# Kernel tuning notes

Hardware: AMD Instinct MI355X
Metric: run time of the kernel (lower is better)

The kernel has to match this reference:

```python
import jax, jax.numpy as jnp
import numpy as np

B, CIN, COUT, K, H, W, MAPPING_DIM = 8, 32, 32, 3, 512, 512, 1024


def setup_inputs() -> dict:
    key = jax.random.key(0)
    k1, k2, k3, k4 = jax.random.split(key, 4)
    x = jax.random.normal(k1, (B, CIN, H, W), dtype=jnp.float32)
    w = jax.random.normal(k2, (B, MAPPING_DIM), dtype=jnp.float32)
    kernel = jax.random.normal(k3, (COUT, CIN, K, K), dtype=jnp.float32) * 0.02
    style_w = jax.random.normal(k4, (CIN, MAPPING_DIM), dtype=jnp.float32) * (1.0 / np.sqrt(MAPPING_DIM))
    style_b = jnp.zeros((CIN,), dtype=jnp.float32)
    return {"x": x, "w": w, "kernel": kernel, "style_w": style_w, "style_b": style_b}


def reference(x, w, kernel, style_w, style_b):
    # style = Linear(MAPPING_DIM -> in_channels)(w)  -> [b, cin]
    style = jnp.einsum('bm,cm->bc', w, style_w) + style_b
    # Per-sample modulated kernel (kernel * style broadcast over input channel)
    # is mathematically identical to scaling input channels then a shared conv:
    # conv(x, kernel * style_b) == conv(x * style_b, kernel). This fuses the
    # modulation into the activations, avoiding the [b*cout, cin, k, k] tensor.
    xm = x * style[:, :, None, None]  # [b, cin, h, w]
    pad = K // 2
    out = jax.lax.conv_general_dilated(
        xm, kernel,
        window_strides=(1, 1),
        padding=[(pad, pad), (pad, pad)],
        dimension_numbers=('NCHW', 'OIHW', 'NCHW'),
    )  # [b, cout, h, w]
    return out
```

## Files before the change

### kernel.cpp

```cpp
#include <hip/hip_runtime.h>
#include <hip/hip_bf16.h>


typedef short  short8 __attribute__((ext_vector_type(8)));
typedef float  f32x4  __attribute__((ext_vector_type(4)));

#define TH 8
#define TW 32
#define XCOLS (TH ? (TW + 2) : 0)
#define CPAD 40

static __device__ inline unsigned short f2bf(float f) {
    unsigned int u = __float_as_uint(f);
    unsigned int r = (u + 0x7fffu + ((u >> 16) & 1u)) >> 16;
    return (unsigned short)r;
}

__global__ void style_kernel(const float* __restrict__ w, const float* __restrict__ sw,
                             const float* __restrict__ sb, float* __restrict__ style) {
    int wid  = (blockIdx.x * 256 + threadIdx.x) >> 6;
    int lane = threadIdx.x & 63;
    int b = wid >> 5, ci = wid & 31;
    const float* wp = w  + b  * 1024;
    const float* sp = sw + ci * 1024;
    float s = 0.f;
    #pragma unroll
    for (int i = 0; i < 16; ++i) s += wp[lane + 64 * i] * sp[lane + 64 * i];
    #pragma unroll
    for (int off = 32; off; off >>= 1) s += __shfl_down(s, off, 64);
    if (lane == 0) style[b * 32 + ci] = s + sb[ci];
}

__global__ void wprep_kernel(const float* __restrict__ kern, const float* __restrict__ style,
                             unsigned short* __restrict__ wfrag) {
    int tid = blockIdx.x * 256 + threadIdx.x;
    if (tid >= 8 * 9216) return;
    int b    = tid / 9216;
    int rem  = tid % 9216;
    int off  = rem >> 10;
    int r2   = rem & 1023;
    int half = r2 >> 9;
    int lane = (r2 >> 3) & 63;
    int j    = r2 & 7;
    int cout = half * 16 + (lane & 15);
    int cin  = (lane >> 4) * 8 + j;
    int kh = off / 3, kw = off % 3;
    float v = kern[(cout * 32 + cin) * 9 + kh * 3 + kw] * style[b * 32 + cin];
    wfrag[tid] = f2bf(v);
}

__global__ __launch_bounds__(256, 4) void conv_kernel(const float* __restrict__ x,
                                                      const unsigned short* __restrict__ wfrag,
                                                      float* __restrict__ out) {
    __shared__ unsigned short xs[(TH + 2) * XCOLS * CPAD];

    const int b  = blockIdx.z;
    const int h0 = blockIdx.y * TH;
    const int w0 = blockIdx.x * TW;
    const int t    = threadIdx.x;
    const int lane = t & 63, wave = t >> 6;

    short8 wreg[9][2];
    const unsigned short* wf = wfrag + b * 9216;
    #pragma unroll
    for (int off = 0; off < 9; ++off)
        #pragma unroll
        for (int hf = 0; hf < 2; ++hf)
            wreg[off][hf] = *(const short8*)(wf + ((off * 2 + hf) * 64 + lane) * 8);

    const float* xb = x + (size_t)b * 8388608;
    for (int tt = t; tt < 1600; tt += 256) {
        int col4 = tt % 10;
        int tmp  = tt / 10;
        int row  = tmp % 10;
        int cp   = tmp / 10;
        int gh   = h0 - 1 + row;
        int gw0  = w0 - 4 + col4 * 4;
        f32x4 a = {0.f, 0.f, 0.f, 0.f};
        f32x4 c = {0.f, 0.f, 0.f, 0.f};
        if ((unsigned)gh < 512u && (unsigned)gw0 <= 508u) {
            const float* p = xb + cp * 2 * 262144 + gh * 512 + gw0;
            a = *(const f32x4*)p;
            c = *(const f32x4*)(p + 262144);
        }
        #pragma unroll
        for (int e = 0; e < 4; ++e) {
            int xcol = col4 * 4 + e - 3;
            if ((unsigned)xcol < (unsigned)XCOLS) {
                float2 fp = make_float2(a[e], c[e]);
                __hip_bfloat162 h2 = __float22bfloat162_rn(fp);
                *(unsigned int*)&xs[(row * XCOLS + xcol) * CPAD + cp * 2] = *(unsigned int*)&h2;
            }
        }
    }
    __syncthreads();

    const int n  = lane & 15;
    const int kg = lane >> 4;
    float* ob = out + (size_t)b * 8388608;

    #pragma unroll 1
    for (int g = 0; g < 4; ++g) {
        const int r   = wave * 2 + (g >> 1);
        const int c16 = (g & 1) * 16;
        f32x4 acc0 = {0.f, 0.f, 0.f, 0.f};
        f32x4 acc1 = {0.f, 0.f, 0.f, 0.f};
        #pragma unroll
        for (int kh = 0; kh < 3; ++kh) {
            #pragma unroll
            for (int kw = 0; kw < 3; ++kw) {
                const short8 afrag =
                    *(const short8*)&xs[((r + kh) * XCOLS + c16 + kw + n) * CPAD + kg * 8];
                const int off = kh * 3 + kw;
                acc0 = __builtin_amdgcn_mfma_f32_16x16x32_bf16(afrag, wreg[off][0], acc0, 0, 0, 0);
                acc1 = __builtin_amdgcn_mfma_f32_16x16x32_bf16(afrag, wreg[off][1], acc1, 0, 0, 0);
            }
        }
        const int gh = h0 + r;
        const int gw = w0 + c16 + kg * 4;
        float* p0 = ob + (size_t)n * 262144 + gh * 512 + gw;
        *(f32x4*)p0 = acc0;
        *(f32x4*)(p0 + 16 * 262144) = acc1;
    }
}

extern "C" void kernel_launch(void* const* d_in, const int* in_sizes, int n_in,
                              void* d_out, int out_size, void* d_ws, size_t ws_size,
                              hipStream_t stream) {
    const float* x    = (const float*)d_in[0];
    const float* w    = (const float*)d_in[1];
    const float* kern = (const float*)d_in[2];
    const float* sw   = (const float*)d_in[3];
    const float* sb   = (const float*)d_in[4];
    float* out = (float*)d_out;

    float*          style = (float*)d_ws;
    unsigned short* wfrag = (unsigned short*)((char*)d_ws + 1024);

    style_kernel<<<64, 256, 0, stream>>>(w, sw, sb, style);
    wprep_kernel<<<288, 256, 0, stream>>>(kern, style, wfrag);
    conv_kernel<<<dim3(512 / TW, 512 / TH, 8), 256, 0, stream>>>(x, wfrag, out);
}
```

Before: 506.5 us.

## Stream rows through a shared-memory ring buffer with prefetch in conv kernel

Each conv block now covers a 64-row by 32-column strip and walks down it eight rows at a time. The next eight input rows are prefetched into registers while MFMA runs on the current rows, then written into a 16-row ring buffer in shared memory, so the halo rows are reused between steps instead of reloaded. The block grows to 512 threads, with each wave pair splitting the output channels. Blocks are remapped to interleave batches, outputs use nontemporal stores, and the style and weight-prep kernels are fused into a single 8-block launch. In exchange there are fewer blocks (1024) and extra barriers, and the prep kernel runs on very few blocks.

```diff
diff --git a/kernel.cpp b/kernel.cpp
--- a/kernel.cpp
+++ b/kernel.cpp
@@ -5,10 +5,9 @@
 typedef short  short8 __attribute__((ext_vector_type(8)));
 typedef float  f32x4  __attribute__((ext_vector_type(4)));
 
-#define TH 8
-#define TW 32
-#define XCOLS (TH ? (TW + 2) : 0)
-#define CPAD 40
+#define XCOLS 34
+#define CPAD  40
+#define NRING 16
 
 static __device__ inline unsigned short f2bf(float f) {
     unsigned int u = __float_as_uint(f);
@@ -16,111 +15,185 @@
     return (unsigned short)r;
 }
 
-__global__ void style_kernel(const float* __restrict__ w, const float* __restrict__ sw,
-                             const float* __restrict__ sb, float* __restrict__ style) {
-    int wid  = (blockIdx.x * 256 + threadIdx.x) >> 6;
-    int lane = threadIdx.x & 63;
-    int b = wid >> 5, ci = wid & 31;
-    const float* wp = w  + b  * 1024;
-    const float* sp = sw + ci * 1024;
-    float s = 0.f;
+__global__ __launch_bounds__(256) void prep_kernel(const float* __restrict__ w,
+                                                   const float* __restrict__ sw,
+                                                   const float* __restrict__ sb,
+                                                   const float* __restrict__ kern,
+                                                   unsigned short* __restrict__ wfrag) {
+    __shared__ float sstyle[32];
+    const int b = blockIdx.x;
+    const int t = threadIdx.x, lane = t & 63, wave = t >> 6;
+    const float* wp = w + b * 1024;
     #pragma unroll
-    for (int i = 0; i < 16; ++i) s += wp[lane + 64 * i] * sp[lane + 64 * i];
+    for (int i = 0; i < 8; ++i) {
+        const int ci = wave * 8 + i;
+        const float* sp = sw + ci * 1024;
+        float s = 0.f;
+        #pragma unroll
+        for (int k = 0; k < 16; ++k) s += wp[lane + 64 * k] * sp[lane + 64 * k];
+        #pragma unroll
+        for (int off = 32; off; off >>= 1) s += __shfl_down(s, off, 64);
+        if (lane == 0) sstyle[ci] = s + sb[ci];
+    }
+    __syncthreads();
+    unsigned short* wfb = wfrag + b * 9216;
     #pragma unroll
-    for (int off = 32; off; off >>= 1) s += __shfl_down(s, off, 64);
-    if (lane == 0) style[b * 32 + ci] = s + sb[ci];
-}
-
-__global__ void wprep_kernel(const float* __restrict__ kern, const float* __restrict__ style,
-                             unsigned short* __restrict__ wfrag) {
-    int tid = blockIdx.x * 256 + threadIdx.x;
-    if (tid >= 8 * 9216) return;
-    int b    = tid / 9216;
-    int rem  = tid % 9216;
-    int off  = rem >> 10;
-    int r2   = rem & 1023;
-    int half = r2 >> 9;
-    int lane = (r2 >> 3) & 63;
-    int j    = r2 & 7;
-    int cout = half * 16 + (lane & 15);
-    int cin  = (lane >> 4) * 8 + j;
-    int kh = off / 3, kw = off % 3;
-    float v = kern[(cout * 32 + cin) * 9 + kh * 3 + kw] * style[b * 32 + cin];
-    wfrag[tid] = f2bf(v);
-}
-
-__global__ __launch_bounds__(256, 4) void conv_kernel(const float* __restrict__ x,
+    for (int k = 0; k < 36; ++k) {
+        const int f = t + 256 * k;
+        const int off = f >> 10, r2 = f & 1023;
+        const int half = r2 >> 9, ln = (r2 >> 3) & 63, j = r2 & 7;
+        const int cout = half * 16 + (ln & 15);
+        const int cin  = (ln >> 4) * 8 + j;
+        const int kh = off / 3, kw = off % 3;
+        wfb[f] = f2bf(kern[(cout * 32 + cin) * 9 + kh * 3 + kw] * sstyle[cin]);
+    }
+}
+
+__global__ __launch_bounds__(512, 4) void conv_kernel(const float* __restrict__ x,
                                                       const unsigned short* __restrict__ wfrag,
                                                       float* __restrict__ out) {
-    __shared__ unsigned short xs[(TH + 2) * XCOLS * CPAD];
-
-    const int b  = blockIdx.z;
-    const int h0 = blockIdx.y * TH;
-    const int w0 = blockIdx.x * TW;
-    const int t    = threadIdx.x;
+    __shared__ unsigned short xs[NRING * XCOLS * CPAD];
+
+    const int p = blockIdx.x;
+    const int q = (p & 7) * 128 + (p >> 3);
+    const int b  = q >> 7;
+    const int tg = (q >> 4) & 7;
+    const int tw = q & 15;
+    const int w0 = tw * 32;
+    const int hbase = tg * 64;
+
+    const int t = threadIdx.x;
     const int lane = t & 63, wave = t >> 6;
-
-    short8 wreg[9][2];
-    const unsigned short* wf = wfrag + b * 9216;
-    #pragma unroll
-    for (int off = 0; off < 9; ++off)
-        #pragma unroll
-        for (int hf = 0; hf < 2; ++hf)
-            wreg[off][hf] = *(const short8*)(wf + ((off * 2 + hf) * 64 + lane) * 8);
+    const int hf = wave & 1;
+    const int ws = wave >> 1;
+    const int n  = lane & 15, kg = lane >> 4;
+
+    short8 wreg[9];
+    {
+        const unsigned short* wf = wfrag + b * 9216;
+        #pragma unroll
+        for (int off = 0; off < 9; ++off)
+            wreg[off] = *(const short8*)(wf + ((off * 2 + hf) * 64 + lane) * 8);
+    }
 
     const float* xb = x + (size_t)b * 8388608;
-    for (int tt = t; tt < 1600; tt += 256) {
-        int col4 = tt % 10;
-        int tmp  = tt / 10;
-        int row  = tmp % 10;
-        int cp   = tmp / 10;
-        int gh   = h0 - 1 + row;
-        int gw0  = w0 - 4 + col4 * 4;
-        f32x4 a = {0.f, 0.f, 0.f, 0.f};
-        f32x4 c = {0.f, 0.f, 0.f, 0.f};
-        if ((unsigned)gh < 512u && (unsigned)gw0 <= 508u) {
-            const float* p = xb + cp * 2 * 262144 + gh * 512 + gw0;
-            a = *(const f32x4*)p;
-            c = *(const f32x4*)(p + 262144);
-        }
-        #pragma unroll
-        for (int e = 0; e < 4; ++e) {
-            int xcol = col4 * 4 + e - 3;
-            if ((unsigned)xcol < (unsigned)XCOLS) {
-                float2 fp = make_float2(a[e], c[e]);
-                __hip_bfloat162 h2 = __float22bfloat162_rn(fp);
-                *(unsigned int*)&xs[(row * XCOLS + xcol) * CPAD + cp * 2] = *(unsigned int*)&h2;
+    float*       ob = out + (size_t)b * 8388608;
+
+    {
+        f32x4 va[4], vc[4];
+        #pragma unroll
+        for (int u = 0; u < 4; ++u) {
+            const int tt = t + 512 * u;
+            va[u] = (f32x4){0.f, 0.f, 0.f, 0.f};
+            vc[u] = (f32x4){0.f, 0.f, 0.f, 0.f};
+            if (tt < 1600) {
+                const int col4 = tt % 10;
+                const int row  = (tt / 10) % 10;
+                const int cp   = tt / 100;
+                const int gh   = hbase - 1 + row;
+                const int gw0  = w0 - 4 + col4 * 4;
+                if ((unsigned)gh < 512u && (unsigned)gw0 <= 508u) {
+                    const float* ptr = xb + cp * 2 * 262144 + gh * 512 + gw0;
+                    va[u] = *(const f32x4*)ptr;
+                    vc[u] = *(const f32x4*)(ptr + 262144);
+                }
+            }
+        }
+        #pragma unroll
+        for (int u = 0; u < 4; ++u) {
+            const int tt = t + 512 * u;
+            if (tt < 1600) {
+                const int col4 = tt % 10;
+                const int row  = (tt / 10) % 10;
+                const int cp   = tt / 100;
+                const int prow = (row + 15) & 15;
+                #pragma unroll
+                for (int e = 0; e < 4; ++e) {
+                    const int xcol = col4 * 4 + e - 3;
+                    if ((unsigned)xcol < (unsigned)XCOLS) {
+                        float2 fp = make_float2(va[u][e], vc[u][e]);
+                        __hip_bfloat162 h2 = __float22bfloat162_rn(fp);
+                        *(unsigned int*)&xs[(prow * XCOLS + xcol) * CPAD + cp * 2] =
+                            *(unsigned int*)&h2;
+                    }
+                }
             }
         }
     }
     __syncthreads();
 
-    const int n  = lane & 15;
-    const int kg = lane >> 4;
-    float* ob = out + (size_t)b * 8388608;
-
     #pragma unroll 1
-    for (int g = 0; g < 4; ++g) {
-        const int r   = wave * 2 + (g >> 1);
-        const int c16 = (g & 1) * 16;
-        f32x4 acc0 = {0.f, 0.f, 0.f, 0.f};
-        f32x4 acc1 = {0.f, 0.f, 0.f, 0.f};
-        #pragma unroll
-        for (int kh = 0; kh < 3; ++kh) {
+    for (int it = 0; it < 8; ++it) {
+        f32x4 va[3], vc[3];
+        const bool more = (it < 7);
+        if (more) {
+            const int grow0 = hbase + it * 8 + 9;
             #pragma unroll
-            for (int kw = 0; kw < 3; ++kw) {
-                const short8 afrag =
-                    *(const short8*)&xs[((r + kh) * XCOLS + c16 + kw + n) * CPAD + kg * 8];
-                const int off = kh * 3 + kw;
-                acc0 = __builtin_amdgcn_mfma_f32_16x16x32_bf16(afrag, wreg[off][0], acc0, 0, 0, 0);
-                acc1 = __builtin_amdgcn_mfma_f32_16x16x32_bf16(afrag, wreg[off][1], acc1, 0, 0, 0);
-            }
-        }
-        const int gh = h0 + r;
-        const int gw = w0 + c16 + kg * 4;
-        float* p0 = ob + (size_t)n * 262144 + gh * 512 + gw;
-        *(f32x4*)p0 = acc0;
-        *(f32x4*)(p0 + 16 * 262144) = acc1;
+            for (int u = 0; u < 3; ++u) {
+                const int tt = t + 512 * u;
+                va[u] = (f32x4){0.f, 0.f, 0.f, 0.f};
+                vc[u] = (f32x4){0.f, 0.f, 0.f, 0.f};
+                if (tt < 1280) {
+                    const int col4 = tt % 10;
+                    const int row  = (tt / 10) % 8;
+                    const int cp   = tt / 80;
+                    const int gh   = grow0 + row;
+                    const int gw0  = w0 - 4 + col4 * 4;
+                    if ((unsigned)gh < 512u && (unsigned)gw0 <= 508u) {
+                        const float* ptr = xb + cp * 2 * 262144 + gh * 512 + gw0;
+                        va[u] = *(const f32x4*)ptr;
+                        vc[u] = *(const f32x4*)(ptr + 262144);
+                    }
+                }
+            }
+        }
+
+        const int base = it * 8;
+        #pragma unroll
+        for (int g = 0; g < 4; ++g) {
+            const int r   = ws * 2 + (g >> 1);
+            const int c16 = (g & 1) * 16;
+            f32x4 acc = {0.f, 0.f, 0.f, 0.f};
+            #pragma unroll
+            for (int kh = 0; kh < 3; ++kh) {
+                const int prow = (base + r + kh - 1) & 15;
+                #pragma unroll
+                for (int kw = 0; kw < 3; ++kw) {
+                    const short8 afrag =
+                        *(const short8*)&xs[(prow * XCOLS + c16 + kw + n) * CPAD + kg * 8];
+                    acc = __builtin_amdgcn_mfma_f32_16x16x32_bf16(afrag, wreg[kh * 3 + kw],
+                                                                  acc, 0, 0, 0);
+                }
+            }
+            const int gh = hbase + base + r;
+            float* p0 = ob + (size_t)(hf * 16 + n) * 262144 + gh * 512 + (w0 + c16 + kg * 4);
+            __builtin_nontemporal_store(acc, (f32x4*)p0);
+        }
+        __syncthreads();
+
+        if (more) {
+            #pragma unroll
+            for (int u = 0; u < 3; ++u) {
+                const int tt = t + 512 * u;
+                if (tt < 1280) {
+                    const int col4 = tt % 10;
+                    const int row  = (tt / 10) % 8;
+                    const int cp   = tt / 80;
+                    const int prow = (it * 8 + 9 + row) & 15;
+                    #pragma unroll
+                    for (int e = 0; e < 4; ++e) {
+                        const int xcol = col4 * 4 + e - 3;
+                        if ((unsigned)xcol < (unsigned)XCOLS) {
+                            float2 fp = make_float2(va[u][e], vc[u][e]);
+                            __hip_bfloat162 h2 = __float22bfloat162_rn(fp);
+                            *(unsigned int*)&xs[(prow * XCOLS + xcol) * CPAD + cp * 2] =
+                                *(unsigned int*)&h2;
+                        }
+                    }
+                }
+            }
+            __syncthreads();
+        }
     }
 }
 
@@ -134,10 +207,8 @@
     const float* sb   = (const float*)d_in[4];
     float* out = (float*)d_out;
 
-    float*          style = (float*)d_ws;
-    unsigned short* wfrag = (unsigned short*)((char*)d_ws + 1024);
-
-    style_kernel<<<64, 256, 0, stream>>>(w, sw, sb, style);
-    wprep_kernel<<<288, 256, 0, stream>>>(kern, style, wfrag);
-    conv_kernel<<<dim3(512 / TW, 512 / TH, 8), 256, 0, stream>>>(x, wfrag, out);
-}
+    unsigned short* wfrag = (unsigned short*)d_ws;
+
+    prep_kernel<<<8, 256, 0, stream>>>(w, sw, sb, kern, wfrag);
+    conv_kernel<<<1024, 512, 0, stream>>>(x, wfrag, out);
+}
```

Measured after the change: 509.6 us. No clear change (+0.6%).

## Pre-transpose input to NHWC bf16 and convolve directly from global memory

Applied to the files above, without the earlier changes.

Adds a pass that converts x into a channels-last bf16 copy (in workspace, or in the spare upper half of the output buffer when workspace is small). The conv kernel then drops its shared-memory staging and reads A fragments straight from the NHWC buffer, with each wave reusing loaded rows for two output rows and owning one half of the output channels. The style and weight-prep kernels are merged into one launch. This trades an extra full read and write of x for contiguous channel loads and no LDS tile or barrier, and the fallback path relies on ordering batches so output writes do not overwrite staged inputs still to be read.

```diff
diff --git a/kernel.cpp b/kernel.cpp
--- a/kernel.cpp
+++ b/kernel.cpp
@@ -5,10 +5,7 @@
 typedef short  short8 __attribute__((ext_vector_type(8)));
 typedef float  f32x4  __attribute__((ext_vector_type(4)));
 
-#define TH 8
-#define TW 32
-#define XCOLS (TH ? (TW + 2) : 0)
-#define CPAD 40
+struct XtBases { unsigned short* p[8]; };
 
 static __device__ inline unsigned short f2bf(float f) {
     unsigned int u = __float_as_uint(f);
@@ -16,111 +13,122 @@
     return (unsigned short)r;
 }
 
-__global__ void style_kernel(const float* __restrict__ w, const float* __restrict__ sw,
-                             const float* __restrict__ sb, float* __restrict__ style) {
-    int wid  = (blockIdx.x * 256 + threadIdx.x) >> 6;
-    int lane = threadIdx.x & 63;
-    int b = wid >> 5, ci = wid & 31;
-    const float* wp = w  + b  * 1024;
-    const float* sp = sw + ci * 1024;
-    float s = 0.f;
+__global__ __launch_bounds__(256) void prep_kernel(const float* __restrict__ w,
+                                                   const float* __restrict__ sw,
+                                                   const float* __restrict__ sb,
+                                                   const float* __restrict__ kern,
+                                                   unsigned short* __restrict__ wfrag) {
+    __shared__ float sstyle[32];
+    const int b = blockIdx.x;
+    const int t = threadIdx.x, lane = t & 63, wave = t >> 6;
+    const float* wp = w + b * 1024;
     #pragma unroll
-    for (int i = 0; i < 16; ++i) s += wp[lane + 64 * i] * sp[lane + 64 * i];
+    for (int i = 0; i < 8; ++i) {
+        const int ci = wave * 8 + i;
+        const float* sp = sw + ci * 1024;
+        float s = 0.f;
+        #pragma unroll
+        for (int k = 0; k < 16; ++k) s += wp[lane + 64 * k] * sp[lane + 64 * k];
+        #pragma unroll
+        for (int off = 32; off; off >>= 1) s += __shfl_down(s, off, 64);
+        if (lane == 0) sstyle[ci] = s + sb[ci];
+    }
+    __syncthreads();
+    unsigned short* wfb = wfrag + b * 9216;
     #pragma unroll
-    for (int off = 32; off; off >>= 1) s += __shfl_down(s, off, 64);
-    if (lane == 0) style[b * 32 + ci] = s + sb[ci];
+    for (int k = 0; k < 36; ++k) {
+        const int f = t + 256 * k;
+        const int off = f >> 10, r2 = f & 1023;
+        const int half = r2 >> 9, ln = (r2 >> 3) & 63, j = r2 & 7;
+        const int cout = half * 16 + (ln & 15);
+        const int cin  = (ln >> 4) * 8 + j;
+        const int kh = off / 3, kw = off % 3;
+        wfb[f] = f2bf(kern[(cout * 32 + cin) * 9 + kh * 3 + kw] * sstyle[cin]);
+    }
 }
 
-__global__ void wprep_kernel(const float* __restrict__ kern, const float* __restrict__ style,
-                             unsigned short* __restrict__ wfrag) {
-    int tid = blockIdx.x * 256 + threadIdx.x;
-    if (tid >= 8 * 9216) return;
-    int b    = tid / 9216;
-    int rem  = tid % 9216;
-    int off  = rem >> 10;
-    int r2   = rem & 1023;
-    int half = r2 >> 9;
-    int lane = (r2 >> 3) & 63;
-    int j    = r2 & 7;
-    int cout = half * 16 + (lane & 15);
-    int cin  = (lane >> 4) * 8 + j;
-    int kh = off / 3, kw = off % 3;
-    float v = kern[(cout * 32 + cin) * 9 + kh * 3 + kw] * style[b * 32 + cin];
-    wfrag[tid] = f2bf(v);
+__global__ __launch_bounds__(256) void xt_kernel(const float* __restrict__ x, XtBases xb) {
+    const int b  = blockIdx.z;
+    const int h  = blockIdx.y;
+    const int w0 = blockIdx.x * 256;
+    const int t   = threadIdx.x;
+    const int px4 = t & 63;
+    const int c8  = t >> 6;
+    const float* xp = x + (size_t)b * 8388608 + h * 512 + (w0 + px4 * 4);
+    f32x4 v[8];
+    #pragma unroll
+    for (int j = 0; j < 8; ++j)
+        v[j] = *(const f32x4*)(xp + (size_t)(c8 * 8 + j) * 262144);
+    unsigned short* o = xb.p[b] + ((size_t)(h * 512 + w0 + px4 * 4) * 32 + c8 * 8);
+    #pragma unroll
+    for (int e = 0; e < 4; ++e) {
+        uint4 d;
+        __hip_bfloat162 h0 = __float22bfloat162_rn(make_float2(v[0][e], v[1][e]));
+        __hip_bfloat162 h1 = __float22bfloat162_rn(make_float2(v[2][e], v[3][e]));
+        __hip_bfloat162 h2 = __float22bfloat162_rn(make_float2(v[4][e], v[5][e]));
+        __hip_bfloat162 h3 = __float22bfloat162_rn(make_float2(v[6][e], v[7][e]));
+        d.x = *(unsigned int*)&h0; d.y = *(unsigned int*)&h1;
+        d.z = *(unsigned int*)&h2; d.w = *(unsigned int*)&h3;
+        *(uint4*)(o + e * 32) = d;
+    }
 }
 
-__global__ __launch_bounds__(256, 4) void conv_kernel(const float* __restrict__ x,
+__global__ __launch_bounds__(256, 4) void conv_kernel(XtBases xb,
                                                       const unsigned short* __restrict__ wfrag,
-                                                      float* __restrict__ out) {
-    __shared__ unsigned short xs[(TH + 2) * XCOLS * CPAD];
+                                                      float* __restrict__ out, int b0) {
+    const int b  = b0 + blockIdx.z;
+    const int h0 = blockIdx.y * 4;
+    const int w0 = blockIdx.x * 32;
+    const int t = threadIdx.x, lane = t & 63, wave = t >> 6;
+    const int hf = wave & 1, rp = wave >> 1;
+    const int n = lane & 15, kg = lane >> 4;
 
-    const int b  = blockIdx.z;
-    const int h0 = blockIdx.y * TH;
-    const int w0 = blockIdx.x * TW;
-    const int t    = threadIdx.x;
-    const int lane = t & 63, wave = t >> 6;
+    short8 wreg[9];
+    {
+        const unsigned short* wf = wfrag + b * 9216;
+        #pragma unroll
+        for (int off = 0; off < 9; ++off)
+            wreg[off] = *(const short8*)(wf + ((off * 2 + hf) * 64 + lane) * 8);
+    }
 
-    short8 wreg[9][2];
-    const unsigned short* wf = wfrag + b * 9216;
+    const unsigned short* xt = xb.p[b];
+    float* ob = out + (size_t)b * 8388608;
+    const int r0 = h0 + rp * 2;
+
     #pragma unroll
-    for (int off = 0; off < 9; ++off)
-        #pragma unroll
-        for (int hf = 0; hf < 2; ++hf)
-            wreg[off][hf] = *(const short8*)(wf + ((off * 2 + hf) * 64 + lane) * 8);
-
-    const float* xb = x + (size_t)b * 8388608;
-    for (int tt = t; tt < 1600; tt += 256) {
-        int col4 = tt % 10;
-        int tmp  = tt / 10;
-        int row  = tmp % 10;
-        int cp   = tmp / 10;
-        int gh   = h0 - 1 + row;
-        int gw0  = w0 - 4 + col4 * 4;
-        f32x4 a = {0.f, 0.f, 0.f, 0.f};
-        f32x4 c = {0.f, 0.f, 0.f, 0.f};
-        if ((unsigned)gh < 512u && (unsigned)gw0 <= 508u) {
-            const float* p = xb + cp * 2 * 262144 + gh * 512 + gw0;
-            a = *(const f32x4*)p;
-            c = *(const f32x4*)(p + 262144);
-        }
-        #pragma unroll
-        for (int e = 0; e < 4; ++e) {
-            int xcol = col4 * 4 + e - 3;
-            if ((unsigned)xcol < (unsigned)XCOLS) {
-                float2 fp = make_float2(a[e], c[e]);
-                __hip_bfloat162 h2 = __float22bfloat162_rn(fp);
-                *(unsigned int*)&xs[(row * XCOLS + xcol) * CPAD + cp * 2] = *(unsigned int*)&h2;
-            }
-        }
-    }
-    __syncthreads();
-
-    const int n  = lane & 15;
-    const int kg = lane >> 4;
-    float* ob = out + (size_t)b * 8388608;
-
-    #pragma unroll 1
-    for (int g = 0; g < 4; ++g) {
-        const int r   = wave * 2 + (g >> 1);
-        const int c16 = (g & 1) * 16;
+    for (int cg = 0; cg < 2; ++cg) {
+        const int c16 = cg * 16;
         f32x4 acc0 = {0.f, 0.f, 0.f, 0.f};
         f32x4 acc1 = {0.f, 0.f, 0.f, 0.f};
         #pragma unroll
-        for (int kh = 0; kh < 3; ++kh) {
-            #pragma unroll
-            for (int kw = 0; kw < 3; ++kw) {
-                const short8 afrag =
-                    *(const short8*)&xs[((r + kh) * XCOLS + c16 + kw + n) * CPAD + kg * 8];
-                const int off = kh * 3 + kw;
-                acc0 = __builtin_amdgcn_mfma_f32_16x16x32_bf16(afrag, wreg[off][0], acc0, 0, 0, 0);
-                acc1 = __builtin_amdgcn_mfma_f32_16x16x32_bf16(afrag, wreg[off][1], acc1, 0, 0, 0);
+        for (int rw = 0; rw < 4; ++rw) {
+            const int grw = r0 + rw - 1;
+            if ((unsigned)grw < 512u) {
+                short8 f[3];
+                #pragma unroll
+                for (int kw = 0; kw < 3; ++kw) {
+                    const int gwf = w0 + c16 + kw - 1;
+                    f[kw] = *(const short8*)(xt + ((grw * 512 + gwf + n) * 32 + kg * 8));
+                    if ((w0 == 0 && c16 == 0 && kw == 0) ||
+                        (w0 == 480 && c16 == 16 && kw == 2)) {
+                        if ((unsigned)(gwf + n) >= 512u)
+                            f[kw] = (short8){0, 0, 0, 0, 0, 0, 0, 0};
+                    }
+                }
+                #pragma unroll
+                for (int kw = 0; kw < 3; ++kw) {
+                    if (rw <= 2)
+                        acc0 = __builtin_amdgcn_mfma_f32_16x16x32_bf16(
+                                   f[kw], wreg[rw * 3 + kw], acc0, 0, 0, 0);
+                    if (rw >= 1)
+                        acc1 = __builtin_amdgcn_mfma_f32_16x16x32_bf16(
+                                   f[kw], wreg[(rw - 1) * 3 + kw], acc1, 0, 0, 0);
+                }
             }
         }
-        const int gh = h0 + r;
-        const int gw = w0 + c16 + kg * 4;
-        float* p0 = ob + (size_t)n * 262144 + gh * 512 + gw;
+        float* p0 = ob + (size_t)(hf * 16 + n) * 262144 + r0 * 512 + (w0 + c16 + kg * 4);
         *(f32x4*)p0 = acc0;
-        *(f32x4*)(p0 + 16 * 262144) = acc1;
+        *(f32x4*)(p0 + 512) = acc1;
     }
 }
 
@@ -134,10 +142,32 @@
     const float* sb   = (const float*)d_in[4];
     float* out = (float*)d_out;
 
-    float*          style = (float*)d_ws;
-    unsigned short* wfrag = (unsigned short*)((char*)d_ws + 1024);
+    unsigned short* wfrag = (unsigned short*)d_ws;
+    const size_t IMG = 16777216;
+    const size_t XT0 = 147520;
+    char* wsp = (char*)d_ws;
+    char* op  = (char*)d_out;
 
-    style_kernel<<<64, 256, 0, stream>>>(w, sw, sb, style);
-    wprep_kernel<<<288, 256, 0, stream>>>(kern, style, wfrag);
-    conv_kernel<<<dim3(512 / TW, 512 / TH, 8), 256, 0, stream>>>(x, wfrag, out);
+    const bool tier1 = ws_size >= XT0 + 8 * IMG + 128;
+    XtBases xb;
+    if (tier1) {
+        for (int b = 0; b < 8; ++b)
+            xb.p[b] = (unsigned short*)(wsp + XT0 + (size_t)b * IMG);
+    } else {
+        for (int b = 0; b < 7; ++b)
+            xb.p[b] = (unsigned short*)(op + 134217728 + (size_t)b * IMG);
+        xb.p[7] = (unsigned short*)(wsp + XT0);
+    }
+
+    prep_kernel<<<8, 256, 0, stream>>>(w, sw, sb, kern, wfrag);
+    xt_kernel<<<dim3(2, 512, 8), 256, 0, stream>>>(x, xb);
+    if (tier1) {
+        conv_kernel<<<dim3(16, 128, 8), 256, 0, stream>>>(xb, wfrag, out, 0);
+    } else {
+        conv_kernel<<<dim3(16, 128, 4), 256, 0, stream>>>(xb, wfrag, out, 0);
+        conv_kernel<<<dim3(16, 128, 1), 256, 0, stream>>>(xb, wfrag, out, 4);
+        conv_kernel<<<dim3(16, 128, 1), 256, 0, stream>>>(xb, wfrag, out, 5);
+        conv_kernel<<<dim3(16, 128, 1), 256, 0, stream>>>(xb, wfrag, out, 6);
+        conv_kernel<<<dim3(16, 128, 1), 256, 0, stream>>>(xb, wfrag, out, 7);
+    }
 }
```

Result: slower. 672.3 us (+32.7%).
